# Kernel optimization log

Hardware: AMD Instinct MI355X
Metric: run time of the kernel (lower is better)

The kernel has to match this reference:

```python
import jax, jax.numpy as jnp
import numpy as np

B, C, H, W, HEADS = 8, 256, 128, 128, 8
HEADC = C // HEADS
EPS = 1e-5


def _ln(t, w, b):
    # per-head LayerNorm over the head-channel dim (last axis),
    # with per-head affine params of shape (heads, 1, headc)
    mu = jnp.mean(t, axis=-1, keepdims=True)
    var = jnp.mean(jnp.square(t - mu), axis=-1, keepdims=True)
    return (t - mu) * jax.lax.rsqrt(var + EPS) * w + b


def _forward(x, w_qkv, b_qkv, kln_w, kln_b, vln_w, vln_b, w_o1, b_o1, w_o2, b_o2):
    b, c, h, w = x.shape
    n = h * w
    heads, headc = kln_w.shape[0], c // kln_w.shape[0]
    # 1x1 conv qkv projection, channels-last output: [b,h,w,3c]
    qkv = jnp.einsum('bchw,oc->bhwo', x, w_qkv) + b_qkv
    qkv = qkv.reshape(b, n, heads, 3 * headc).transpose(0, 2, 1, 3)  # [b,heads,n,3*headc]
    q, k, v = jnp.split(qkv, 3, axis=-1)  # each [b,heads,n,headc]
    k = _ln(k, kln_w, kln_b)
    v = _ln(v, vln_w, vln_b)
    # Galerkin linear attention: (k^T v) then q @ (k^T v), normalized by n
    kv = jnp.einsum('bhnd,bhne->bhde', k, v) / n  # [b,heads,headc,headc]
    att = jnp.einsum('bhnd,bhde->bhne', q, kv)    # [b,heads,n,headc]
    att = att.transpose(0, 2, 1, 3).reshape(b, h, w, c).transpose(0, 3, 1, 2)
    ret = att + x
    y = jnp.einsum('bchw,oc->bohw', ret, w_o1) + b_o1[None, :, None, None]
    y = jax.nn.gelu(y, approximate=False)  # torch nn.GELU default = exact erf
    y = jnp.einsum('bchw,oc->bohw', y, w_o2) + b_o2[None, :, None, None]
    return y + x


def setup_inputs() -> dict:
    key = jax.random.key(0)
    ks = jax.random.split(key, 4)
    return {
        'x': jax.random.normal(ks[0], (B, C, H, W), dtype=jnp.float32),
        'w_qkv': jax.random.normal(ks[1], (3 * C, C), dtype=jnp.float32) * 0.02,
        'b_qkv': jnp.zeros((3 * C,), dtype=jnp.float32),
        'kln_w': jnp.ones((HEADS, 1, HEADC), dtype=jnp.float32),
        'kln_b': jnp.zeros((HEADS, 1, HEADC), dtype=jnp.float32),
        'vln_w': jnp.ones((HEADS, 1, HEADC), dtype=jnp.float32),
        'vln_b': jnp.zeros((HEADS, 1, HEADC), dtype=jnp.float32),
        'w_o1': jax.random.normal(ks[2], (C, C), dtype=jnp.float32) * 0.02,
        'b_o1': jnp.zeros((C,), dtype=jnp.float32),
        'w_o2': jax.random.normal(ks[3], (C, C), dtype=jnp.float32) * 0.02,
        'b_o2': jnp.zeros((C,), dtype=jnp.float32),
    }


def reference(x, w_qkv, b_qkv, kln_w, kln_b, vln_w, vln_b, w_o1, b_o1, w_o2, b_o2):
    return _forward(x, w_qkv, b_qkv, kln_w, kln_b, vln_w, vln_b, w_o1, b_o1, w_o2, b_o2)
```

## Files before the change

kernel.cpp:

```cpp
#include <hip/hip_runtime.h>
#include <hip/hip_bf16.h>
#include <cstdint>

typedef unsigned short u16;
typedef __attribute__((ext_vector_type(8))) short short8;
typedef __attribute__((ext_vector_type(4))) short short4v;
typedef __attribute__((ext_vector_type(4))) float f32x4;

#define HW_N 16384
#define CCH  256
#define BATCH 8
#define NHEAD 8
#define HEADC 32

static __device__ __forceinline__ float bf2f(u16 u){
    union { float f; uint32_t i; } x; x.i = ((uint32_t)u) << 16; return x.f;
}
static __device__ __forceinline__ u16 f2bf(float f){
    union { float f; uint32_t i; } x; x.f = f;
    uint32_t r = x.i + 0x7fffu + ((x.i >> 16) & 1u);
    return (u16)(r >> 16);
}

#define GLD16(gp, lp) __builtin_amdgcn_global_load_lds( \
    (const __attribute__((address_space(1))) uint32_t*)(gp), \
    (__attribute__((address_space(3))) uint32_t*)(lp), 16, 0, 0)

__global__ __launch_bounds__(256) void k_transpose_cast(const float* __restrict__ x,
                                                        u16* __restrict__ xb){
    __shared__ float tile[64][65];
    int b = blockIdx.z, ct = blockIdx.y, nt = blockIdx.x;
    int t = threadIdx.x;
    const float* src = x + ((size_t)b * CCH + ct * 64) * HW_N + nt * 64;
    #pragma unroll
    for (int it = 0; it < 16; ++it){
        int f = it * 256 + t;
        int i = f >> 6, j = f & 63;
        tile[i][j] = src[(size_t)i * HW_N + j];
    }
    __syncthreads();
    u16* dst = xb + ((size_t)b * HW_N + nt * 64) * CCH + ct * 64;
    #pragma unroll
    for (int it = 0; it < 16; ++it){
        int f = it * 256 + t;
        int jj = f >> 6, ii = f & 63;
        dst[(size_t)jj * CCH + ii] = f2bf(tile[ii][jj]);
    }
}

__global__ __launch_bounds__(256) void k_weight_prep(const float* __restrict__ w_qkv,
                                                     const float* __restrict__ b_qkv,
                                                     const float* __restrict__ w_o1,
                                                     const float* __restrict__ w_o2,
                                                     u16* __restrict__ wkv_b,
                                                     float* __restrict__ bkv_re,
                                                     u16* __restrict__ w_o1_b,
                                                     u16* __restrict__ w_o2_b){
    int id = blockIdx.x * 256 + threadIdx.x;
    if (id < 512 * 256){
        int r = id >> 8, c = id & 255;
        int h = r >> 6, s = (r >> 5) & 1, d = r & 31;
        int srow = h * 96 + 32 + s * 32 + d;
        wkv_b[id] = f2bf(w_qkv[(size_t)srow * 256 + c]);
        if (c == 0) bkv_re[r] = b_qkv[srow];
    } else {
        int id2 = id - 512 * 256;
        if (id2 < 65536)       w_o1_b[id2]         = f2bf(w_o1[id2]);
        else if (id2 < 131072) w_o2_b[id2 - 65536] = f2bf(w_o2[id2 - 65536]);
    }
}

__global__ __launch_bounds__(256, 2) void k_gemm_kv(const u16* __restrict__ A,
                                                    const u16* __restrict__ Bt,
                                                    const float* __restrict__ bkv,
                                                    const float* __restrict__ kln_w,
                                                    const float* __restrict__ kln_b,
                                                    const float* __restrict__ vln_w,
                                                    const float* __restrict__ vln_b,
                                                    float* __restrict__ kvpart){
    __shared__ __align__(16) u16 sh[16384];
    u16* lsA = sh;
    u16* lsB = sh + 8192;

    int lin = blockIdx.x + 4 * (blockIdx.y + 128 * blockIdx.z);
    int bx = (lin >> 3) & 3;
    int rest = (lin & 7) | ((lin >> 5) << 3);
    int by = rest & 127;
    int bz = rest >> 7;

    int row0 = bz * HW_N + by * 128;
    int col0 = bx * 128;

    int t = threadIdx.x;
    int wid = t >> 6, lane = t & 63;
    int wr = wid >> 1, wc = wid & 1;
    int q = lane >> 4, q4 = q * 4, lrow = lane & 15;

    f32x4 acc[4][4];
    #pragma unroll
    for (int i = 0; i < 4; ++i)
        #pragma unroll
        for (int j = 0; j < 4; ++j) acc[i][j] = (f32x4)0.0f;

    for (int kt = 0; kt < 4; ++kt){
        int c0 = kt * 64;
        #pragma unroll
        for (int it = 0; it < 4; ++it){
            int f  = it * 256 + t;
            int fs = f ^ ((f >> 3) & 7);
            int r  = f >> 3, c8 = (fs & 7) * 8;
            GLD16(&A [((size_t)(row0 + r)) * 256 + c0 + c8], &lsA[f * 8]);
            GLD16(&Bt[((size_t)(col0 + r)) * 256 + c0 + c8], &lsB[f * 8]);
        }
        __syncthreads();
        #pragma unroll
        for (int ks = 0; ks < 2; ++ks){
            int lk = q * 8 + ks * 32;
            short8 af[4], bfr[4];
            #pragma unroll
            for (int mi = 0; mi < 4; ++mi){
                int row = wr * 64 + mi * 16 + lrow;
                int e = (row * 64 + lk) ^ ((row & 7) << 3);
                af[mi] = *(const short8*)&lsA[e];
            }
            #pragma unroll
            for (int ni = 0; ni < 4; ++ni){
                int row = wc * 64 + ni * 16 + lrow;
                int e = (row * 64 + lk) ^ ((row & 7) << 3);
                bfr[ni] = *(const short8*)&lsB[e];
            }
            #pragma unroll
            for (int mi = 0; mi < 4; ++mi)
                #pragma unroll
                for (int ni = 0; ni < 4; ++ni)
                    acc[mi][ni] = __builtin_amdgcn_mfma_f32_16x16x32_bf16(
                        bfr[ni], af[mi], acc[mi][ni], 0, 0, 0);
        }
        __syncthreads();
    }

    int h = 2 * bx + wc;
    float bv[4][4], lwv[4][4], lbv[4][4];
    #pragma unroll
    for (int ni = 0; ni < 4; ++ni){
        const float* w  = (ni < 2) ? kln_w : vln_w;
        const float* bb = (ni < 2) ? kln_b : vln_b;
        #pragma unroll
        for (int r = 0; r < 4; ++r){
            int de = (ni & 1) * 16 + q4 + r;
            bv[ni][r]  = bkv[col0 + wc * 64 + ni * 16 + q4 + r];
            lwv[ni][r] = w[h * 32 + de];
            lbv[ni][r] = bb[h * 32 + de];
        }
    }

    #pragma unroll
    for (int mi = 0; mi < 4; ++mi){
        float ks = 0.f, ksq = 0.f, vs = 0.f, vsq = 0.f;
        #pragma unroll
        for (int ni = 0; ni < 4; ++ni)
            #pragma unroll
            for (int r = 0; r < 4; ++r){
                float t2 = acc[mi][ni][r] + bv[ni][r];
                acc[mi][ni][r] = t2;
                if (ni < 2){ ks += t2; ksq += t2 * t2; }
                else       { vs += t2; vsq += t2 * t2; }
            }
        ks  += __shfl_xor(ks, 16);  ks  += __shfl_xor(ks, 32);
        ksq += __shfl_xor(ksq, 16); ksq += __shfl_xor(ksq, 32);
        vs  += __shfl_xor(vs, 16);  vs  += __shfl_xor(vs, 32);
        vsq += __shfl_xor(vsq, 16); vsq += __shfl_xor(vsq, 32);
        float muk = ks * 0.03125f, muv = vs * 0.03125f;
        float rsk = rsqrtf(fmaxf(ksq * 0.03125f - muk * muk, 0.f) + 1e-5f);
        float rsv = rsqrtf(fmaxf(vsq * 0.03125f - muv * muv, 0.f) + 1e-5f);
        int n = wr * 64 + mi * 16 + lrow;
        #pragma unroll
        for (int ni = 0; ni < 4; ++ni){
            float mu = (ni < 2) ? muk : muv;
            float rs = (ni < 2) ? rsk : rsv;
            #pragma unroll
            for (int r = 0; r < 4; ++r){
                int d = (ni & 1) * 16 + q4 + r;
                float val = (acc[mi][ni][r] - mu) * rs * lwv[ni][r] + lbv[ni][r];
                int byteoff = ((wc * 2 + (ni >> 1)) << 13) + (d << 8) + (n << 1);
                byteoff ^= (d & 7) << 4;
                *(u16*)((char*)sh + byteoff) = f2bf(val);
            }
        }
    }
    __syncthreads();

    if (wid < 2){
        f32x4 a2[2][2];
        #pragma unroll
        for (int i = 0; i < 2; ++i)
            #pragma unroll
            for (int j = 0; j < 2; ++j) a2[i][j] = (f32x4)0.0f;
        #pragma unroll
        for (int ks2 = 0; ks2 < 4; ++ks2){
            int n0 = q * 8 + ks2 * 32;
            short8 kf[2], vf[2];
            #pragma unroll
            for (int mi = 0; mi < 2; ++mi){
                int d = mi * 16 + lrow;
                int bko = ((wid * 2 + 0) << 13) + (d << 8) + (n0 << 1);
                int bvo = ((wid * 2 + 1) << 13) + (d << 8) + (n0 << 1);
                bko ^= (d & 7) << 4;
                bvo ^= (d & 7) << 4;
                kf[mi] = *(const short8*)((char*)sh + bko);
                vf[mi] = *(const short8*)((char*)sh + bvo);
            }
            #pragma unroll
            for (int mi = 0; mi < 2; ++mi)
                #pragma unroll
                for (int ni = 0; ni < 2; ++ni)
                    a2[mi][ni] = __builtin_amdgcn_mfma_f32_16x16x32_bf16(
                        kf[mi], vf[ni], a2[mi][ni], 0, 0, 0);
        }
        float* dst = kvpart + (((size_t)(bz * 128 + by)) * 8 + 2 * bx + wid) * 1024;
        #pragma unroll
        for (int mi = 0; mi < 2; ++mi)
            #pragma unroll
            for (int ni = 0; ni < 2; ++ni)
                #pragma unroll
                for (int r = 0; r < 4; ++r)
                    dst[(mi * 16 + q4 + r) * 32 + ni * 16 + lrow] = a2[mi][ni][r];
    }
}

__global__ __launch_bounds__(256) void k_wqeff(const float* __restrict__ kvpart,
                                               const float* __restrict__ w_qkv,
                                               const float* __restrict__ b_qkv,
                                               u16* __restrict__ wq_eff_b,
                                               float* __restrict__ beff){
    __shared__ float kv[1024];
    int h = blockIdx.x, b = blockIdx.y;
    int t = threadIdx.x;
    f32x4 s = (f32x4)0.0f;
    for (int p = 0; p < 128; ++p){
        f32x4 v = *(const f32x4*)(kvpart + (((size_t)b * 128 + p) * 8 + h) * 1024 + t * 4);
        s = s + v;
    }
    const float invN = 1.0f / (float)HW_N;
    #pragma unroll
    for (int i = 0; i < 4; ++i) kv[t * 4 + i] = s[i] * invN;
    __syncthreads();

    float wcol[32];
    #pragma unroll
    for (int d = 0; d < 32; ++d)
        wcol[d] = w_qkv[((size_t)(h * 96 + d)) * 256 + t];
    for (int e = 0; e < 32; ++e){
        float s2 = 0.f;
        #pragma unroll
        for (int d = 0; d < 32; ++d) s2 += wcol[d] * kv[d * 32 + e];
        wq_eff_b[(((size_t)b * 256) + h * 32 + e) * 256 + t] = f2bf(s2);
    }
    if (t < 32){
        float s3 = 0.f;
        #pragma unroll
        for (int d = 0; d < 32; ++d) s3 += b_qkv[h * 96 + d] * kv[d * 32 + t];
        beff[b * 256 + h * 32 + t] = s3;
    }
}

#define STAGE_B(BT, KT, BUF) do {                                             \
    _Pragma("unroll")                                                         \
    for (int it_ = 0; it_ < 4; ++it_){                                        \
        int f_ = it_ * 256 + t;                                               \
        int o_ = f_ >> 2, sl_ = f_ & 3;                                       \
        GLD16(&(BT)[(size_t)o_ * 256 + (KT) * 32 + (sl_ ^ (o_ & 3)) * 8],     \
              &(BUF)[f_ * 8]);                                                \
    }                                                                         \
} while(0)

#define ZACC do {                                                             \
    _Pragma("unroll") for (int i_ = 0; i_ < 4; ++i_)                          \
    _Pragma("unroll") for (int j_ = 0; j_ < 4; ++j_)                          \
        acc[i_][j_] = (f32x4)0.0f;                                            \
} while(0)

#define KLOOP(BT, SWAPPED) do {                                               \
    for (int kt = 0; kt < 8; ++kt){                                           \
        int cur = kt & 1;                                                     \
        if (kt < 7) STAGE_B(BT, kt + 1, Bs[cur ^ 1]);                         \
        short8 af[4], bf[4];                                                  \
        _Pragma("unroll")                                                     \
        for (int mi = 0; mi < 4; ++mi){                                       \
            int n_ = mi * 16 + lrow;                                          \
            int sl_ = (kt * 4 + q) ^ (n_ & 7);                                \
            af[mi] = *(const short8*)((const char*)I + n_ * 512 + (sl_ << 4));\
        }                                                                     \
        _Pragma("unroll")                                                     \
        for (int ni = 0; ni < 4; ++ni){                                       \
            int o_ = wid * 64 + ni * 16 + lrow;                               \
            bf[ni] = *(const short8*)((const char*)Bs[cur] + o_ * 64          \
                                      + ((q ^ (o_ & 3)) << 4));               \
        }                                                                     \
        _Pragma("unroll")                                                     \
        for (int mi = 0; mi < 4; ++mi)                                        \
            _Pragma("unroll")                                                 \
            for (int ni = 0; ni < 4; ++ni)                                    \
                acc[mi][ni] = (SWAPPED)                                       \
                    ? __builtin_amdgcn_mfma_f32_16x16x32_bf16(                \
                          bf[ni], af[mi], acc[mi][ni], 0, 0, 0)               \
                    : __builtin_amdgcn_mfma_f32_16x16x32_bf16(                \
                          af[mi], bf[ni], acc[mi][ni], 0, 0, 0);              \
        __syncthreads();                                                      \
    }                                                                         \
} while(0)

__global__ __launch_bounds__(256, 2) void k_fused3(const u16* __restrict__ xb,
                                                   const u16* __restrict__ wq_effb,
                                                   const float* __restrict__ beff,
                                                   const u16* __restrict__ w_o1_b,
                                                   const float* __restrict__ b_o1,
                                                   const u16* __restrict__ w_o2_b,
                                                   const float* __restrict__ b_o2,
                                                   const float* __restrict__ x,
                                                   float* __restrict__ out){
    __shared__ __align__(16) u16 I[16384];
    __shared__ __align__(16) u16 Bs[2][8192];

    int d = blockIdx.x;
    int bz = d & 7, nb = d >> 3;
    size_t row0 = (size_t)bz * HW_N + (size_t)nb * 64;

    int t = threadIdx.x, wid = t >> 6, lane = t & 63;
    int lrow = lane & 15, q = lane >> 4, q4 = q * 4;

    const u16* B1 = wq_effb + (size_t)bz * 65536;

    #pragma unroll
    for (int it = 0; it < 8; ++it){
        int f = it * 256 + t;
        int n = f >> 5, slot = f & 31;
        GLD16(&xb[(row0 + n) * 256 + (size_t)((slot ^ (n & 7)) * 8)], &I[f * 8]);
    }
    STAGE_B(B1, 0, Bs[0]);
    __syncthreads();

    f32x4 acc[4][4];

    ZACC;
    KLOOP(B1, true);
    STAGE_B(w_o1_b, 0, Bs[0]);
    #pragma unroll
    for (int ni = 0; ni < 4; ++ni){
        int o0 = wid * 64 + ni * 16 + q4;
        f32x4 be = *(const f32x4*)&beff[bz * 256 + o0];
        #pragma unroll
        for (int mi = 0; mi < 4; ++mi){
            int n = mi * 16 + lrow;
            int byte = (n * 512 + o0 * 2) ^ ((n & 7) << 4);
            short4v rv = *(const short4v*)((const char*)I + byte);
            short4v pk;
            #pragma unroll
            for (int r = 0; r < 4; ++r)
                pk[r] = (short)f2bf(acc[mi][ni][r] + be[r] + bf2f((u16)rv[r]));
            *(short4v*)((char*)I + byte) = pk;
        }
    }
    __syncthreads();

    ZACC;
    KLOOP(w_o1_b, true);
    STAGE_B(w_o2_b, 0, Bs[0]);
    #pragma unroll
    for (int ni = 0; ni < 4; ++ni){
        int o0 = wid * 64 + ni * 16 + q4;
        f32x4 bo = *(const f32x4*)&b_o1[o0];
        #pragma unroll
        for (int mi = 0; mi < 4; ++mi){
            int n = mi * 16 + lrow;
            int byte = (n * 512 + o0 * 2) ^ ((n & 7) << 4);
            short4v pk;
            #pragma unroll
            for (int r = 0; r < 4; ++r){
                float v = acc[mi][ni][r] + bo[r];
                v = 0.5f * v * (1.0f + erff(v * 0.70710678118654752f));
                pk[r] = (short)f2bf(v);
            }
            *(short4v*)((char*)I + byte) = pk;
        }
    }
    __syncthreads();

    ZACC;
    KLOOP(w_o2_b, false);
    #pragma unroll
    for (int ni = 0; ni < 4; ++ni){
        int o = wid * 64 + ni * 16 + lrow;
        float bo = b_o2[o];
        size_t base = ((size_t)bz * 256 + o) * HW_N + (size_t)nb * 64;
        #pragma unroll
        for (int mi = 0; mi < 4; ++mi){
            int n0 = mi * 16 + q4;
            f32x4 xv = *(const f32x4*)&x[base + n0];
            f32x4 ov;
            #pragma unroll
            for (int r = 0; r < 4; ++r) ov[r] = acc[mi][ni][r] + bo + xv[r];
            *(f32x4*)&out[base + n0] = ov;
        }
    }
}

extern "C" void kernel_launch(void* const* d_in, const int* in_sizes, int n_in,
                              void* d_out, int out_size, void* d_ws, size_t ws_size,
                              hipStream_t stream){
    const float* x     = (const float*)d_in[0];
    const float* w_qkv = (const float*)d_in[1];
    const float* b_qkv = (const float*)d_in[2];
    const float* kln_w = (const float*)d_in[3];
    const float* kln_b = (const float*)d_in[4];
    const float* vln_w = (const float*)d_in[5];
    const float* vln_b = (const float*)d_in[6];
    const float* w_o1  = (const float*)d_in[7];
    const float* b_o1  = (const float*)d_in[8];
    const float* w_o2  = (const float*)d_in[9];
    const float* b_o2  = (const float*)d_in[10];
    float* out = (float*)d_out;

    const size_t MB = 1u << 20;
    if (ws_size < 266 * MB) return;

    char* ws = (char*)d_ws;
    u16*   xb      = (u16*)(ws);
    float* kvpart  = (float*)(ws + 192 * MB);
    char*  sm      = ws + 264 * MB;
    u16*   wkv_b   = (u16*)sm;
    float* bkv_re  = (float*)(sm + 256 * 1024);
    u16*   w_o1_b  = (u16*)(sm + 260 * 1024);
    u16*   w_o2_b  = (u16*)(sm + 392 * 1024);
    u16*   wq_effb = (u16*)(sm + 524 * 1024);
    float* beff    = (float*)(sm + 1572 * 1024);

    k_transpose_cast<<<dim3(HW_N / 64, CCH / 64, BATCH), 256, 0, stream>>>(x, xb);
    k_weight_prep<<<dim3(1024), 256, 0, stream>>>(w_qkv, b_qkv, w_o1, w_o2,
                                                  wkv_b, bkv_re, w_o1_b, w_o2_b);
    k_gemm_kv<<<dim3(4, 128, BATCH), 256, 0, stream>>>(
        xb, wkv_b, bkv_re, kln_w, kln_b, vln_w, vln_b, kvpart);
    k_wqeff<<<dim3(NHEAD, BATCH), 256, 0, stream>>>(kvpart, w_qkv, b_qkv, wq_effb, beff);
    k_fused3<<<dim3(2048), 256, 0, stream>>>(
        xb, wq_effb, beff, w_o1_b, b_o1, w_o2_b, b_o2, x, out);
}
```

Measured before the change: 250.5 us.

## Replace __syncthreads in GEMM k-loops with explicit vmcnt waits and raw barriers

The three chained GEMM k-loops are rewritten. Each uses an explicit s_waitcnt vmcnt(4) or vmcnt(0) plus s_barrier instead of full __syncthreads, so the prefetch of the next B tile can stay in flight while the current tile is consumed. B-fragment LDS reads are moved ahead of A reads, the MFMA block is wrapped in s_setprio, and the loop is fully unrolled. Epilogue barriers become lgkmcnt(0)+s_barrier. The goal is less full-drain synchronisation and better overlap of global-to-LDS loads with MFMA. The cost is fragile hand-counted wait counts that depend on the exact number of outstanding loads.

After: 249.3 us. About the same (-0.5%).

```diff
diff --git a/kernel.cpp b/kernel.cpp
--- a/kernel.cpp
+++ b/kernel.cpp
@@ -280,23 +280,32 @@
         acc[i_][j_] = (f32x4)0.0f;                                            \
 } while(0)
 
-#define KLOOP(BT, SWAPPED) do {                                               \
+#define GEMM_STAGE_PIPE(BT, SWAPPED) do {                                     \
+    _Pragma("unroll")                                                         \
     for (int kt = 0; kt < 8; ++kt){                                           \
         int cur = kt & 1;                                                     \
-        if (kt < 7) STAGE_B(BT, kt + 1, Bs[cur ^ 1]);                         \
+        if (kt < 7){                                                          \
+            STAGE_B(BT, kt + 1, Bs[cur ^ 1]);                                 \
+            asm volatile("s_waitcnt vmcnt(4)" ::: "memory");                  \
+        } else {                                                              \
+            asm volatile("s_waitcnt vmcnt(0)" ::: "memory");                  \
+        }                                                                     \
+        __builtin_amdgcn_s_barrier();                                         \
+        __builtin_amdgcn_sched_barrier(0);                                    \
         short8 af[4], bf[4];                                                  \
+        _Pragma("unroll")                                                     \
+        for (int ni = 0; ni < 4; ++ni){                                       \
+            int o_ = wid * 64 + ni * 16 + lrow;                               \
+            bf[ni] = *(const short8*)((const char*)Bs[cur] + o_ * 64          \
+                                      + ((q ^ (o_ & 3)) << 4));               \
+        }                                                                     \
         _Pragma("unroll")                                                     \
         for (int mi = 0; mi < 4; ++mi){                                       \
             int n_ = mi * 16 + lrow;                                          \
             int sl_ = (kt * 4 + q) ^ (n_ & 7);                                \
             af[mi] = *(const short8*)((const char*)I + n_ * 512 + (sl_ << 4));\
         }                                                                     \
-        _Pragma("unroll")                                                     \
-        for (int ni = 0; ni < 4; ++ni){                                       \
-            int o_ = wid * 64 + ni * 16 + lrow;                               \
-            bf[ni] = *(const short8*)((const char*)Bs[cur] + o_ * 64          \
-                                      + ((q ^ (o_ & 3)) << 4));               \
-        }                                                                     \
+        __builtin_amdgcn_s_setprio(1);                                        \
         _Pragma("unroll")                                                     \
         for (int mi = 0; mi < 4; ++mi)                                        \
             _Pragma("unroll")                                                 \
@@ -306,8 +315,15 @@
                           bf[ni], af[mi], acc[mi][ni], 0, 0, 0)               \
                     : __builtin_amdgcn_mfma_f32_16x16x32_bf16(                \
                           af[mi], bf[ni], acc[mi][ni], 0, 0, 0);              \
-        __syncthreads();                                                      \
+        __builtin_amdgcn_s_setprio(0);                                        \
+        __builtin_amdgcn_s_barrier();                                         \
     }                                                                         \
+} while(0)
+
+#define LDS_FENCE_BARRIER() do {                                              \
+    asm volatile("s_waitcnt lgkmcnt(0)" ::: "memory");                        \
+    __builtin_amdgcn_s_barrier();                                             \
+    __builtin_amdgcn_sched_barrier(0);                                        \
 } while(0)
 
 __global__ __launch_bounds__(256, 2) void k_fused3(const u16* __restrict__ xb,
@@ -338,12 +354,11 @@
         GLD16(&xb[(row0 + n) * 256 + (size_t)((slot ^ (n & 7)) * 8)], &I[f * 8]);
     }
     STAGE_B(B1, 0, Bs[0]);
-    __syncthreads();
 
     f32x4 acc[4][4];
 
     ZACC;
-    KLOOP(B1, true);
+    GEMM_STAGE_PIPE(B1, true);
     STAGE_B(w_o1_b, 0, Bs[0]);
     #pragma unroll
     for (int ni = 0; ni < 4; ++ni){
@@ -361,10 +376,10 @@
             *(short4v*)((char*)I + byte) = pk;
         }
     }
-    __syncthreads();
+    LDS_FENCE_BARRIER();
 
     ZACC;
-    KLOOP(w_o1_b, true);
+    GEMM_STAGE_PIPE(w_o1_b, true);
     STAGE_B(w_o2_b, 0, Bs[0]);
     #pragma unroll
     for (int ni = 0; ni < 4; ++ni){
@@ -384,10 +399,10 @@
             *(short4v*)((char*)I + byte) = pk;
         }
     }
-    __syncthreads();
+    LDS_FENCE_BARRIER();
 
     ZACC;
-    KLOOP(w_o2_b, false);
+    GEMM_STAGE_PIPE(w_o2_b, false);
     #pragma unroll
     for (int ni = 0; ni < 4; ++ni){
         int o = wid * 64 + ni * 16 + lrow;
```
